# Kernel optimization log

Measured on AMD Instinct MI355X. Metric: run time of the kernel, lower is better.

## Reference

```python
import jax, jax.numpy as jnp
import numpy as np

N_NODES = 8192
GNN_DIM = 512
N_FEAT = 64
N_ITER = 4


def setup_inputs() -> dict:
    key = jax.random.key(0)
    ks = jax.random.split(key, 8)
    scale = 1.0 / np.sqrt(GNN_DIM)
    return {
        "labels": jax.random.normal(ks[0], (N_NODES, GNN_DIM), dtype=jnp.float32),
        "adj": jax.random.uniform(ks[1], (N_NODES, N_NODES), dtype=jnp.float32),
        "features": jax.random.normal(ks[2], (N_FEAT,), dtype=jnp.float32),
        "W_self": jax.random.normal(ks[3], (GNN_DIM, GNN_DIM), dtype=jnp.float32) * scale,
        "b_self": jax.random.normal(ks[4], (GNN_DIM,), dtype=jnp.float32) * scale,
        "W_neigh": jax.random.normal(ks[5], (GNN_DIM, GNN_DIM), dtype=jnp.float32) * scale,
        "W_fc": jax.random.normal(ks[6], (1, GNN_DIM + N_FEAT), dtype=jnp.float32) * scale,
        "b_fc": jax.random.normal(ks[7], (1,), dtype=jnp.float32) * scale,
    }


def reference(labels, adj, features, W_self, b_self, W_neigh, W_fc, b_fc):
    x = labels  # [N, D]
    for _ in range(N_ITER):
        acc = adj @ x                                   # [N, D] neighbor aggregation
        x = jax.nn.relu(x @ W_self.T + b_self + acc @ W_neigh.T)
    pooled = jnp.mean(x, axis=0)                        # [D]
    z = jnp.concatenate([pooled, features]) @ W_fc.T + b_fc  # [1]
    return jax.nn.sigmoid(z)
```

## Files before the change

kernel.cpp:

```cpp
#include <hip/hip_runtime.h>

typedef __bf16 bf16;
typedef bf16 bf16x8 __attribute__((ext_vector_type(8)));
typedef bf16 bf16x4 __attribute__((ext_vector_type(4)));
typedef float f32x4 __attribute__((ext_vector_type(4)));

constexpr int NN = 8192;
constexpr int DD = 512;
constexpr size_t PSZB = (size_t)NN * DD * 2;
constexpr size_t PSZE = (size_t)NN * DD;
constexpr int NS = 4;

static __device__ inline bf16x8 cvt8(const float* __restrict__ p) {
  f32x4 a = *(const f32x4*)p;
  f32x4 b = *(const f32x4*)(p + 4);
  bf16x8 r;
  r[0] = (bf16)a[0]; r[1] = (bf16)a[1]; r[2] = (bf16)a[2]; r[3] = (bf16)a[3];
  r[4] = (bf16)b[0]; r[5] = (bf16)b[1]; r[6] = (bf16)b[2]; r[7] = (bf16)b[3];
  return r;
}

#define GLDS(g, l) __builtin_amdgcn_global_load_lds( \
    (const __attribute__((address_space(1))) unsigned int*)(const void*)(g), \
    (__attribute__((address_space(3))) unsigned int*)(void*)(l), 16, 0, 0)


__global__ __launch_bounds__(256) void convert_w_kernel(
    const float* __restrict__ a, const float* __restrict__ b,
    bf16* __restrict__ ao, bf16* __restrict__ bo) {
  int i8 = ((int)blockIdx.x * 256 + (int)threadIdx.x) * 8;
  if (i8 < DD * DD) {
    *(bf16x8*)&ao[i8] = cvt8(a + i8);
  } else {
    int j = i8 - DD * DD;
    *(bf16x8*)&bo[j] = cvt8(b + j);
  }
}

__global__ __launch_bounds__(256) void convert_adj_kernel(
    const float* __restrict__ a, bf16* __restrict__ o) {
  size_t i8 = ((size_t)blockIdx.x * 256 + threadIdx.x) * 8;
  *(bf16x8*)&o[i8] = cvt8(a + i8);
}

__global__ __launch_bounds__(256) void convert_x_kernel(
    const float* __restrict__ src, bf16* __restrict__ xb, bf16* __restrict__ xbT) {
  __shared__ __align__(16) float tile[64][68];
  const int tid = (int)threadIdx.x;
  const int r0 = (int)blockIdx.x * 64;
  const int c0 = (int)blockIdx.y * 64;
#pragma unroll
  for (int p = 0; p < 4; ++p) {
    int row = p * 16 + (tid >> 4);
    int col = (tid & 15) * 4;
    *(f32x4*)&tile[row][col] = *(const f32x4*)&src[(size_t)(r0 + row) * DD + c0 + col];
  }
  __syncthreads();
#pragma unroll
  for (int p = 0; p < 4; ++p) {
    int row = p * 16 + (tid >> 4);
    int col = (tid & 15) * 4;
    f32x4 v = *(const f32x4*)&tile[row][col];
    bf16x4 o;
    o[0] = (bf16)v[0]; o[1] = (bf16)v[1]; o[2] = (bf16)v[2]; o[3] = (bf16)v[3];
    *(bf16x4*)&xb[(size_t)(r0 + row) * DD + c0 + col] = o;
  }
  {
    int c = tid >> 2;
    int rp = (tid & 3) * 16;
    bf16x8 o0, o1;
#pragma unroll
    for (int j = 0; j < 8; ++j) o0[j] = (bf16)tile[rp + j][c];
#pragma unroll
    for (int j = 0; j < 8; ++j) o1[j] = (bf16)tile[rp + 8 + j][c];
    *(bf16x8*)&xbT[(size_t)(c0 + c) * NN + r0 + rp] = o0;
    *(bf16x8*)&xbT[(size_t)(c0 + c) * NN + r0 + rp + 8] = o1;
  }
}


__device__ __forceinline__ void stage_half(const bf16* __restrict__ g, int grow0, int k0,
                                           bf16* smbase, int wave, int lane) {
#pragma unroll
  for (int i = 0; i < 2; ++i) {
    int c = wave * 2 + i;
    int row = grow0 + c * 8 + (lane >> 3);
    int col = k0 + (((lane & 7) ^ ((lane >> 3) & 7)) << 3);
    GLDS(g + (size_t)row * NN + col, smbase + c * 512);
  }
}

__global__ __launch_bounds__(512, 2)
void gemm1_kernel(const bf16* __restrict__ adjb, const bf16* __restrict__ xbT,
                  bf16* __restrict__ pbase) {
  __shared__ __align__(16) bf16 sm[65536];
  const int bid  = (int)blockIdx.x;
  const int xcd  = bid & 7, ii = bid >> 3;
  const int cb   = ii & 1;
  const int jj_  = xcd + 8 * (ii >> 1);
  const int p    = jj_ >> 2;
  const int s    = jj_ & 3;
  const int prow0 = p * 256;
  const int bcol0 = cb * 256;
  const int kb    = s * 2048;
  bf16* __restrict__ P = pbase + (size_t)s * PSZE;

  const int tid  = (int)threadIdx.x;
  const int lane = tid & 63;
  const int wave = tid >> 6;
  const int wr   = wave >> 2;
  const int wc   = wave & 3;
  const int fr   = lane & 15, fq = lane >> 4;

  f32x4 acc[8][4] = {};

#define A_OFF(par) ((par) * 32768)
#define B_OFF(par) ((par) * 32768 + 16384)
#define STAGE_A(tile, half, par) \
  stage_half(adjb, prow0 + (half) * 128, kb + ((tile) & 31) * 64, \
             sm + A_OFF(par) + (half) * 8192, wave, lane)
#define STAGE_B(tile, half, par) \
  stage_half(xbT, bcol0 + (half) * 128, kb + ((tile) & 31) * 64, \
             sm + B_OFF(par) + (half) * 8192, wave, lane)

  STAGE_B(0, 0, 0); STAGE_B(0, 1, 0); STAGE_A(0, 0, 0);
  STAGE_A(0, 1, 0); STAGE_B(1, 0, 1); STAGE_B(1, 1, 1); STAGE_A(1, 0, 1);

  bf16x8 bv[2][4], af[2][2];

#define LOAD_B(par)                                                        \
  _Pragma("unroll") for (int kk = 0; kk < 2; ++kk)                         \
  _Pragma("unroll") for (int n = 0; n < 4; ++n) {                          \
    int rowl = wc * 64 + n * 16 + fr;                                      \
    int slot = (kk * 4 + fq) ^ (rowl & 7);                                 \
    bv[kk][n] = *(const bf16x8*)&sm[B_OFF(par) + rowl * 64 + slot * 8];    \
  }
#define LOAD_A(q, par)                                                     \
  _Pragma("unroll") for (int kk = 0; kk < 2; ++kk)                         \
  _Pragma("unroll") for (int j = 0; j < 2; ++j) {                          \
    int rowl = (q) * 64 + wr * 32 + j * 16 + fr;                           \
    int slot = (kk * 4 + fq) ^ (rowl & 7);                                 \
    af[kk][j] = *(const bf16x8*)&sm[A_OFF(par) + rowl * 64 + slot * 8];    \
  }
#define QMFMA(q)                                                           \
  _Pragma("unroll") for (int kk = 0; kk < 2; ++kk)                         \
  _Pragma("unroll") for (int j = 0; j < 2; ++j)                            \
  _Pragma("unroll") for (int n = 0; n < 4; ++n)                            \
    acc[2 * (q) + j][n] = __builtin_amdgcn_mfma_f32_16x16x32_bf16(         \
        af[kk][j], bv[kk][n], acc[2 * (q) + j][n], 0, 0, 0);
#define PHASE_TAIL(q)                                                      \
  __builtin_amdgcn_s_barrier();                                            \
  asm volatile("s_waitcnt lgkmcnt(0)" ::: "memory");                       \
  __builtin_amdgcn_sched_barrier(0);                                       \
  __builtin_amdgcn_s_setprio(1);                                           \
  QMFMA(q);                                                                \
  __builtin_amdgcn_s_setprio(0);                                           \
  __builtin_amdgcn_s_barrier();

  for (int it = 0; it < 16; ++it) {
    const int t = it * 2;
    asm volatile("s_waitcnt vmcnt(8)" ::: "memory");
    LOAD_B(0);
    LOAD_A(0, 0);
    STAGE_A(t + 1, 1, 1);
    PHASE_TAIL(0);
    LOAD_A(1, 0);
    STAGE_B(t + 2, 0, 0);
    PHASE_TAIL(1);
    asm volatile("s_waitcnt vmcnt(10)" ::: "memory");
    LOAD_A(2, 0);
    STAGE_B(t + 2, 1, 0);
    PHASE_TAIL(2);
    LOAD_A(3, 0);
    STAGE_A(t + 2, 0, 0);
    PHASE_TAIL(3);
    asm volatile("s_waitcnt vmcnt(8)" ::: "memory");
    LOAD_B(1);
    LOAD_A(0, 1);
    STAGE_A(t + 2, 1, 0);
    PHASE_TAIL(0);
    LOAD_A(1, 1);
    STAGE_B(t + 3, 0, 1);
    PHASE_TAIL(1);
    asm volatile("s_waitcnt vmcnt(10)" ::: "memory");
    LOAD_A(2, 1);
    STAGE_B(t + 3, 1, 1);
    PHASE_TAIL(2);
    LOAD_A(3, 1);
    STAGE_A(t + 3, 0, 1);
    PHASE_TAIL(3);
  }

#pragma unroll
  for (int m = 0; m < 8; ++m)
#pragma unroll
    for (int n = 0; n < 4; ++n)
#pragma unroll
      for (int r = 0; r < 4; ++r) {
        int row = prow0 + (m >> 1) * 64 + wr * 32 + (m & 1) * 16 + fq * 4 + r;
        int col = bcol0 + wc * 64 + n * 16 + fr;
        P[(size_t)row * DD + col] = (bf16)acc[m][n][r];
      }
#undef A_OFF
#undef B_OFF
#undef STAGE_A
#undef STAGE_B
#undef LOAD_B
#undef LOAD_A
#undef QMFMA
#undef PHASE_TAIL
}

__global__ __launch_bounds__(1024, 4)
void gemm2_kernel(const bf16* __restrict__ wsb, const bf16* __restrict__ wnb,
                  bf16* __restrict__ xb, const bf16* __restrict__ pbase,
                  const float* __restrict__ bself, bf16* __restrict__ xbT) {
  __shared__ __align__(16) char smem[139264];
  const int tid  = (int)threadIdx.x;
  const int lane = tid & 63;
  const int wave = tid >> 6;
  const int n0 = (int)blockIdx.x * 32;
  const int fr = lane & 15, fq = lane >> 4;
  const int srow = lane >> 3;
  const int scol = ((lane & 7) ^ (srow & 7)) * 8;
  const int fnode = tid >> 3, fks = tid & 7;

  f32x4 acc[2][2] = {};

  {
    bf16* la = (bf16*)smem;
#pragma unroll
    for (int c = 0; c < 4; ++c) {
      int chunk = wave * 4 + c;
      GLDS(wsb + (size_t)(chunk * 8 + srow) * DD + scol, &la[chunk * 512]);
    }
    if (wave < 4)
      GLDS(xb + (size_t)(n0 + wave * 8 + srow) * DD + scol,
           &((bf16*)(smem + 131072))[wave * 512]);
  }
  asm volatile("s_waitcnt vmcnt(0)" ::: "memory");
  __builtin_amdgcn_s_barrier();

  for (int t = 0; t < 16; ++t) {
    const int par = t & 1;
    bf16* la = (bf16*)(smem + par * 65536);
    bf16* lb = (bf16*)(smem + 131072 + par * 4096);

    bf16x8 fv0, fv1, fv2, fv3;
    bool fold = false;
    if (t < 15) {
      const int tn = t + 1, prn = tn >> 3, k0n = (tn & 7) * 64;
      const bf16* __restrict__ An = prn ? wnb : wsb;
      bf16* lan = (bf16*)(smem + (par ^ 1) * 65536);
#pragma unroll
      for (int c = 0; c < 4; ++c) {
        int chunk = wave * 4 + c;
        GLDS(An + (size_t)(chunk * 8 + srow) * DD + k0n + scol, &lan[chunk * 512]);
      }
      if (prn == 0) {
        if (wave < 4)
          GLDS(xb + (size_t)(n0 + wave * 8 + srow) * DD + k0n + scol,
               &((bf16*)(smem + 131072 + (par ^ 1) * 4096))[wave * 512]);
      } else if (tid < 256) {
        fold = true;
        const bf16* p0 = pbase + (size_t)(n0 + fnode) * DD + k0n + fks * 8;
        fv0 = *(const bf16x8*)(p0);
        fv1 = *(const bf16x8*)(p0 + PSZE);
        fv2 = *(const bf16x8*)(p0 + 2 * PSZE);
        fv3 = *(const bf16x8*)(p0 + 3 * PSZE);
      }
    }

    bf16x8 af[2][2], bv[2][2];
#pragma unroll
    for (int kk = 0; kk < 2; ++kk) {
#pragma unroll
      for (int m = 0; m < 2; ++m) {
        int rowl = wave * 32 + m * 16 + fr;
        int slot = (kk * 4 + fq) ^ (rowl & 7);
        af[kk][m] = *(const bf16x8*)&la[rowl * 64 + slot * 8];
      }
#pragma unroll
      for (int n = 0; n < 2; ++n) {
        int rowl = n * 16 + fr;
        int slot = (kk * 4 + fq) ^ (rowl & 7);
        bv[kk][n] = *(const bf16x8*)&lb[rowl * 64 + slot * 8];
      }
    }
#pragma unroll
    for (int kk = 0; kk < 2; ++kk)
#pragma unroll
      for (int m = 0; m < 2; ++m)
#pragma unroll
        for (int n = 0; n < 2; ++n)
          acc[m][n] = __builtin_amdgcn_mfma_f32_16x16x32_bf16(af[kk][m], bv[kk][n], acc[m][n], 0, 0, 0);

    if (fold) {
      bf16x8 o;
#pragma unroll
      for (int j = 0; j < 8; ++j)
        o[j] = (bf16)((float)fv0[j] + (float)fv1[j] + (float)fv2[j] + (float)fv3[j]);
      *(bf16x8*)&((bf16*)(smem + 131072 + (par ^ 1) * 4096))[fnode * 64 + (fks ^ (fnode & 7)) * 8] = o;
    }

    asm volatile("s_waitcnt vmcnt(0) lgkmcnt(0)" ::: "memory");
    __builtin_amdgcn_s_barrier();
  }

  bf16* lds_t = (bf16*)smem;
#pragma unroll
  for (int m = 0; m < 2; ++m)
#pragma unroll
    for (int n = 0; n < 2; ++n)
#pragma unroll
      for (int r = 0; r < 4; ++r) {
        int d = wave * 32 + m * 16 + fq * 4 + r;
        int node = n * 16 + fr;
        float v = acc[m][n][r] + bself[d];
        v = v > 0.f ? v : 0.f;
        bf16 h = (bf16)v;
        xbT[(size_t)d * NN + n0 + node] = h;
        lds_t[node * 520 + d] = h;
      }
  __syncthreads();
  {
    int node = tid >> 5;
    int dc = (tid & 31) * 16;
    bf16x8 v0 = *(const bf16x8*)&lds_t[node * 520 + dc];
    bf16x8 v1 = *(const bf16x8*)&lds_t[node * 520 + dc + 8];
    *(bf16x8*)&xb[(size_t)(n0 + node) * DD + dc] = v0;
    *(bf16x8*)&xb[(size_t)(n0 + node) * DD + dc + 8] = v1;
  }
}


__global__ __launch_bounds__(256) void pool_kernel(
    const bf16* __restrict__ xb, float* __restrict__ pooled) {
  const int t = (int)threadIdx.x;
  const int r0 = (int)blockIdx.x * 32;
  float s0 = 0.f, s1 = 0.f;
  for (int r = 0; r < 32; ++r) {
    s0 += (float)xb[(size_t)(r0 + r) * DD + t];
    s1 += (float)xb[(size_t)(r0 + r) * DD + t + 256];
  }
  atomicAdd(&pooled[t], s0);
  atomicAdd(&pooled[t + 256], s1);
}

__global__ __launch_bounds__(64) void final_kernel(
    const float* __restrict__ pooled, const float* __restrict__ features,
    const float* __restrict__ wfc, const float* __restrict__ bfc,
    float* __restrict__ out) {
  const int t = (int)threadIdx.x;
  float s = 0.f;
  for (int i = t; i < DD + 64; i += 64) {
    float v = (i < DD) ? pooled[i] * (1.0f / (float)NN) : features[i - DD];
    s += v * wfc[i];
  }
#pragma unroll
  for (int off = 32; off > 0; off >>= 1) s += __shfl_down(s, off);
  if (t == 0) {
    float z = s + bfc[0];
    out[0] = 1.0f / (1.0f + expf(-z));
  }
}


extern "C" void kernel_launch(void* const* d_in, const int* in_sizes, int n_in,
                              void* d_out, int out_size, void* d_ws, size_t ws_size,
                              hipStream_t stream) {
  const float* labels   = (const float*)d_in[0];
  const float* adj      = (const float*)d_in[1];
  const float* features = (const float*)d_in[2];
  const float* W_self   = (const float*)d_in[3];
  const float* b_self   = (const float*)d_in[4];
  const float* W_neigh  = (const float*)d_in[5];
  const float* W_fc     = (const float*)d_in[6];
  const float* b_fc     = (const float*)d_in[7];
  float* out = (float*)d_out;

  char* ws = (char*)d_ws;
  bf16*  xb    = (bf16*)(ws);
  bf16*  xbT   = (bf16*)(ws + PSZB);
  bf16*  pbase = (bf16*)(ws + 2 * PSZB);
  char*  after_p = ws + (size_t)(2 + NS) * PSZB;
  bf16*  wsb    = (bf16*)(after_p);
  bf16*  wnb    = (bf16*)(after_p + 524288);
  float* pooled = (float*)(after_p + 1048576);
  bf16*  adjb   = (bf16*)(after_p + 1048576 + 4096);

  convert_w_kernel<<<2 * DD * DD / 8 / 256, 256, 0, stream>>>(W_self, W_neigh, wsb, wnb);
  convert_adj_kernel<<<(int)((size_t)NN * NN / 8 / 256), 256, 0, stream>>>(adj, adjb);
  convert_x_kernel<<<dim3(NN / 64, DD / 64), 256, 0, stream>>>(labels, xb, xbT);

  for (int it = 0; it < 4; ++it) {
    gemm1_kernel<<<256, 512, 0, stream>>>(adjb, xbT, pbase);
    gemm2_kernel<<<NN / 32, 1024, 0, stream>>>(wsb, wnb, xb, pbase, b_self, xbT);
  }

  hipMemsetAsync(pooled, 0, DD * sizeof(float), stream);
  pool_kernel<<<NN / 32, 256, 0, stream>>>(xb, pooled);
  final_kernel<<<1, 64, 0, stream>>>(pooled, features, W_fc, b_fc, out);
}
```

Measured before the change: 411.8 us.

## Fuse mean-pool into last gemm2, coalesce gemm1 stores via LDS, retune vmcnt waits

```diff
diff --git a/kernel.cpp b/kernel.cpp
--- a/kernel.cpp
+++ b/kernel.cpp
@@ -125,6 +125,7 @@
 
   STAGE_B(0, 0, 0); STAGE_B(0, 1, 0); STAGE_A(0, 0, 0);
   STAGE_A(0, 1, 0); STAGE_B(1, 0, 1); STAGE_B(1, 1, 1); STAGE_A(1, 0, 1);
+  asm volatile("s_waitcnt vmcnt(8)" ::: "memory");
 
   bf16x8 bv[2][4], af[2][2];
 
@@ -148,6 +149,7 @@
   _Pragma("unroll") for (int n = 0; n < 4; ++n)                            \
     acc[2 * (q) + j][n] = __builtin_amdgcn_mfma_f32_16x16x32_bf16(         \
         af[kk][j], bv[kk][n], acc[2 * (q) + j][n], 0, 0, 0);
+#define VMC(N) asm volatile("s_waitcnt vmcnt(" #N ")" ::: "memory")
 #define PHASE_TAIL(q)                                                      \
   __builtin_amdgcn_s_barrier();                                            \
   asm volatile("s_waitcnt lgkmcnt(0)" ::: "memory");                       \
@@ -159,48 +161,63 @@
 
   for (int it = 0; it < 16; ++it) {
     const int t = it * 2;
-    asm volatile("s_waitcnt vmcnt(8)" ::: "memory");
-    LOAD_B(0);
-    LOAD_A(0, 0);
+    LOAD_B(0); LOAD_A(0, 0);
     STAGE_A(t + 1, 1, 1);
     PHASE_TAIL(0);
     LOAD_A(1, 0);
     STAGE_B(t + 2, 0, 0);
+    VMC(10);
     PHASE_TAIL(1);
-    asm volatile("s_waitcnt vmcnt(10)" ::: "memory");
     LOAD_A(2, 0);
     STAGE_B(t + 2, 1, 0);
     PHASE_TAIL(2);
     LOAD_A(3, 0);
     STAGE_A(t + 2, 0, 0);
+    VMC(8);
     PHASE_TAIL(3);
-    asm volatile("s_waitcnt vmcnt(8)" ::: "memory");
-    LOAD_B(1);
-    LOAD_A(0, 1);
+    LOAD_B(1); LOAD_A(0, 1);
     STAGE_A(t + 2, 1, 0);
     PHASE_TAIL(0);
     LOAD_A(1, 1);
     STAGE_B(t + 3, 0, 1);
+    VMC(10);
     PHASE_TAIL(1);
-    asm volatile("s_waitcnt vmcnt(10)" ::: "memory");
     LOAD_A(2, 1);
     STAGE_B(t + 3, 1, 1);
     PHASE_TAIL(2);
     LOAD_A(3, 1);
     STAGE_A(t + 3, 0, 1);
+    VMC(8);
     PHASE_TAIL(3);
   }
 
-#pragma unroll
-  for (int m = 0; m < 8; ++m)
-#pragma unroll
-    for (int n = 0; n < 4; ++n)
-#pragma unroll
-      for (int r = 0; r < 4; ++r) {
-        int row = prow0 + (m >> 1) * 64 + wr * 32 + (m & 1) * 16 + fq * 4 + r;
-        int col = bcol0 + wc * 64 + n * 16 + fr;
-        P[(size_t)row * DD + col] = (bf16)acc[m][n][r];
-      }
+  asm volatile("s_waitcnt vmcnt(0)" ::: "memory");
+  __builtin_amdgcn_s_barrier();
+  {
+    bf16* lt = sm;
+    const int trow = tid >> 2;
+    const int tc0  = (tid & 3) * 64;
+#pragma unroll
+    for (int pass = 0; pass < 2; ++pass) {
+#pragma unroll
+      for (int m2 = 0; m2 < 4; ++m2) {
+        int m = pass * 4 + m2;
+        int rbase = ((m >> 1) * 64 + wr * 32 + (m & 1) * 16 + fq * 4) - pass * 128;
+#pragma unroll
+        for (int n = 0; n < 4; ++n)
+#pragma unroll
+          for (int r = 0; r < 4; ++r)
+            lt[(rbase + r) * 264 + wc * 64 + n * 16 + fr] = (bf16)acc[m][n][r];
+      }
+      __builtin_amdgcn_s_barrier();
+#pragma unroll
+      for (int j = 0; j < 8; ++j) {
+        bf16x8 v = *(const bf16x8*)&lt[trow * 264 + tc0 + j * 8];
+        *(bf16x8*)&P[(size_t)(prow0 + pass * 128 + trow) * DD + bcol0 + tc0 + j * 8] = v;
+      }
+      __builtin_amdgcn_s_barrier();
+    }
+  }
 #undef A_OFF
 #undef B_OFF
 #undef STAGE_A
@@ -208,13 +225,15 @@
 #undef LOAD_B
 #undef LOAD_A
 #undef QMFMA
+#undef VMC
 #undef PHASE_TAIL
 }
 
 __global__ __launch_bounds__(1024, 4)
 void gemm2_kernel(const bf16* __restrict__ wsb, const bf16* __restrict__ wnb,
                   bf16* __restrict__ xb, const bf16* __restrict__ pbase,
-                  const float* __restrict__ bself, bf16* __restrict__ xbT) {
+                  const float* __restrict__ bself, bf16* __restrict__ xbT,
+                  float* __restrict__ pooled, int dopool) {
   __shared__ __align__(16) char smem[139264];
   const int tid  = (int)threadIdx.x;
   const int lane = tid & 63;
@@ -308,6 +327,7 @@
   }
 
   bf16* lds_t = (bf16*)smem;
+  float vv[2][2][4];
 #pragma unroll
   for (int m = 0; m < 2; ++m)
 #pragma unroll
@@ -318,10 +338,27 @@
         int node = n * 16 + fr;
         float v = acc[m][n][r] + bself[d];
         v = v > 0.f ? v : 0.f;
+        vv[m][n][r] = v;
         bf16 h = (bf16)v;
         xbT[(size_t)d * NN + n0 + node] = h;
         lds_t[node * 520 + d] = h;
       }
+  if (dopool) {
+#pragma unroll
+    for (int m = 0; m < 2; ++m)
+#pragma unroll
+      for (int r = 0; r < 4; ++r) {
+        float sv = vv[m][0][r] + vv[m][1][r];
+        sv += __shfl_xor(sv, 1);
+        sv += __shfl_xor(sv, 2);
+        sv += __shfl_xor(sv, 4);
+        sv += __shfl_xor(sv, 8);
+        if (fr == 0) {
+          int d = wave * 32 + m * 16 + fq * 4 + r;
+          atomicAdd(&pooled[d], sv);
+        }
+      }
+  }
   __syncthreads();
   {
     int node = tid >> 5;
@@ -333,19 +370,6 @@
   }
 }
 
-
-__global__ __launch_bounds__(256) void pool_kernel(
-    const bf16* __restrict__ xb, float* __restrict__ pooled) {
-  const int t = (int)threadIdx.x;
-  const int r0 = (int)blockIdx.x * 32;
-  float s0 = 0.f, s1 = 0.f;
-  for (int r = 0; r < 32; ++r) {
-    s0 += (float)xb[(size_t)(r0 + r) * DD + t];
-    s1 += (float)xb[(size_t)(r0 + r) * DD + t + 256];
-  }
-  atomicAdd(&pooled[t], s0);
-  atomicAdd(&pooled[t + 256], s1);
-}
 
 __global__ __launch_bounds__(64) void final_kernel(
     const float* __restrict__ pooled, const float* __restrict__ features,
@@ -389,16 +413,16 @@
   float* pooled = (float*)(after_p + 1048576);
   bf16*  adjb   = (bf16*)(after_p + 1048576 + 4096);
 
+  hipMemsetAsync(pooled, 0, DD * sizeof(float), stream);
   convert_w_kernel<<<2 * DD * DD / 8 / 256, 256, 0, stream>>>(W_self, W_neigh, wsb, wnb);
   convert_adj_kernel<<<(int)((size_t)NN * NN / 8 / 256), 256, 0, stream>>>(adj, adjb);
   convert_x_kernel<<<dim3(NN / 64, DD / 64), 256, 0, stream>>>(labels, xb, xbT);
 
   for (int it = 0; it < 4; ++it) {
     gemm1_kernel<<<256, 512, 0, stream>>>(adjb, xbT, pbase);
-    gemm2_kernel<<<NN / 32, 1024, 0, stream>>>(wsb, wnb, xb, pbase, b_self, xbT);
-  }
-
-  hipMemsetAsync(pooled, 0, DD * sizeof(float), stream);
-  pool_kernel<<<NN / 32, 256, 0, stream>>>(xb, pooled);
+    gemm2_kernel<<<NN / 32, 1024, 0, stream>>>(wsb, wnb, xb, pbase, b_self, xbT,
+                                               pooled, it == 3 ? 1 : 0);
+  }
+
   final_kernel<<<1, 64, 0, stream>>>(pooled, features, W_fc, b_fc, out);
 }
```

Result: slower. 449.8 us (+9.2%).
